# Kernel tuning notes

Hardware: AMD Instinct MI355X
Metric: run time of the kernel (lower is better)

Reference implementation:

```python
import jax, jax.numpy as jnp
import numpy as np
from jax import lax

B, P, ENC = 64, 196, 2048
E, H, A, V = 512, 512, 512, 10000
L = 21  # caption length -> T = 20 decode steps


def setup_inputs() -> dict:
    key = jax.random.key(0)
    ks = jax.random.split(key, 20)
    s = 0.02
    inp = {
        "features": jax.random.normal(ks[0], (B, P, ENC), jnp.float32),
        "captions": jax.random.randint(ks[1], (B, L), 0, V),
        # attention
        "W_enc_att": jax.random.normal(ks[2], (ENC, A), jnp.float32) * s,
        "b_enc_att": jnp.zeros((A,), jnp.float32),
        "W_dec_att": jax.random.normal(ks[3], (H, A), jnp.float32) * s,
        "b_dec_att": jnp.zeros((A,), jnp.float32),
        "W_full": jax.random.normal(ks[4], (A, 1), jnp.float32) * s,
        "b_full": jnp.zeros((1,), jnp.float32),
        # embedding (uniform(-0.1, 0.1) as in init_weights)
        "emb": jax.random.uniform(ks[5], (V, E), jnp.float32, -0.1, 0.1),
        # LSTMCell: input = embed + encoder_dim, gate order i,f,g,o
        "W_ih": jax.random.normal(ks[6], (E + ENC, 4 * H), jnp.float32) * s,
        "W_hh": jax.random.normal(ks[7], (H, 4 * H), jnp.float32) * s,
        "b_ih": jnp.zeros((4 * H,), jnp.float32),
        "b_hh": jnp.zeros((4 * H,), jnp.float32),
        # init state projections
        "W_init_h": jax.random.normal(ks[8], (ENC, H), jnp.float32) * s,
        "b_init_h": jnp.zeros((H,), jnp.float32),
        "W_init_c": jax.random.normal(ks[9], (ENC, H), jnp.float32) * s,
        "b_init_c": jnp.zeros((H,), jnp.float32),
        # gating
        "W_fbeta": jax.random.normal(ks[10], (H, ENC), jnp.float32) * s,
        "b_fbeta": jnp.zeros((ENC,), jnp.float32),
        # output fc (uniform(-0.1,0.1), bias 0)
        "W_fc": jax.random.uniform(ks[11], (H, V), jnp.float32, -0.1, 0.1),
        "b_fc": jnp.zeros((V,), jnp.float32),
    }
    return inp


def reference(features, captions, W_enc_att, b_enc_att, W_dec_att, b_dec_att,
              W_full, b_full, emb, W_ih, W_hh, b_ih, b_hh,
              W_init_h, b_init_h, W_init_c, b_init_c,
              W_fbeta, b_fbeta, W_fc, b_fc):
    # init hidden state from mean-pooled encoder features
    mean_enc = features.mean(axis=1)                       # [B, ENC]
    h0 = mean_enc @ W_init_h + b_init_h                    # [B, H]
    c0 = mean_enc @ W_init_c + b_init_c

    # encoder-side attention projection is time-invariant: precompute
    att1 = features @ W_enc_att + b_enc_att                # [B, P, A]

    T = captions.shape[1] - 1                              # decode_lengths = L-1 (equal lengths)
    embs = emb[captions[:, :T]]                            # [B, T, E]
    embs_t = jnp.swapaxes(embs, 0, 1)                      # [T, B, E]

    def step(carry, e_t):
        h, c = carry
        att2 = h @ W_dec_att + b_dec_att                   # [B, A]
        scores = (jax.nn.relu(att1 + att2[:, None, :]) @ W_full)[..., 0] + b_full  # [B, P]
        alpha = jax.nn.softmax(scores, axis=1)
        awe = jnp.einsum('bp,bpe->be', alpha, features)    # [B, ENC]
        gate = jax.nn.sigmoid(h @ W_fbeta + b_fbeta)
        awe = gate * awe
        x = jnp.concatenate([e_t, awe], axis=1)            # [B, E+ENC]
        gates = x @ W_ih + h @ W_hh + b_ih + b_hh          # [B, 4H]
        i, f, g, o = jnp.split(gates, 4, axis=1)
        c_new = jax.nn.sigmoid(f) * c + jax.nn.sigmoid(i) * jnp.tanh(g)
        h_new = jax.nn.sigmoid(o) * jnp.tanh(c_new)
        preds = h_new @ W_fc + b_fc                        # dropout in eval mode = identity
        return (h_new, c_new), preds

    _, preds = lax.scan(step, (h0, c0), embs_t)            # [T, B, V]
    return jnp.swapaxes(preds, 0, 1)                       # [B, T, V]
```

## Files before the change

### kernel.cpp

```cpp
#include <hip/hip_runtime.h>
#include <hip/hip_bf16.h>


#define TB 256

typedef __bf16 bf16x8 __attribute__((ext_vector_type(8)));
typedef float f32x4 __attribute__((ext_vector_type(4)));
typedef unsigned short u16x8 __attribute__((ext_vector_type(8)));
typedef unsigned short u16x4 __attribute__((ext_vector_type(4)));
typedef unsigned short ushort_t;

__device__ __forceinline__ ushort_t f2bf(float x) {
    unsigned u = __builtin_bit_cast(unsigned, x);
    u += 0x7fffu + ((u >> 16) & 1u);
    return (ushort_t)(u >> 16);
}
__device__ __forceinline__ float bf2f(ushort_t b) {
    return __builtin_bit_cast(float, (unsigned)b << 16);
}
__device__ __forceinline__ void store_pack(
    ushort_t* __restrict__ Ph, ushort_t* __restrict__ Pl,
    int KC, int m, int k, float v)
{
    const size_t flat = ((((size_t)(m >> 4) * KC + (k >> 5)) * 64)
                         + ((k & 31) >> 3) * 16 + (m & 15)) * 8 + (k & 7);
    const ushort_t h = f2bf(v);
    Ph[flat] = h;
    Pl[flat] = f2bf(v - bf2f(h));
}

struct PackJobs {
    const float* W[7];
    ushort_t* Bh[7];
    ushort_t* Bl[7];
    int Nsrc[7], ntCount[7], KC[7], ntBase[7];
    int cum[8];
};

__global__ __launch_bounds__(TB) void pack_all(PackJobs J)
{
    const int blk = blockIdx.x;
    int j = 0;
    #pragma unroll
    for (int i = 1; i < 7; ++i) if (blk >= J.cum[i]) j = i;
    const int g = (blk - J.cum[j]) * TB + threadIdx.x;
    const int KC = J.KC[j];
    const int lane = g & 63;
    const int kc = (g >> 6) % KC;
    const int nt = g / (64 * KC);
    if (nt >= J.ntCount[j]) return;
    const int Nsrc = J.Nsrc[j];
    const float* W = J.W[j];
    const int n = nt * 16 + (lane & 15);
    const int kb = kc * 32 + (lane >> 4) * 8;
    u16x8 hv, lv;
    #pragma unroll
    for (int e = 0; e < 8; ++e) {
        const float x = (n < Nsrc) ? W[(size_t)(kb + e) * Nsrc + n] : 0.f;
        const ushort_t h = f2bf(x);
        hv[e] = h;
        lv[e] = f2bf(x - bf2f(h));
    }
    const size_t flat = (((size_t)(J.ntBase[j] + nt) * KC + kc) * 64 + lane) * 8;
    *(u16x8*)&J.Bh[j][flat] = hv;
    *(u16x8*)&J.Bl[j][flat] = lv;
}

__global__ __launch_bounds__(TB) void feat2bf(
    const float* __restrict__ f, ushort_t* __restrict__ fbf)
{
    const size_t i8 = ((size_t)blockIdx.x * TB + threadIdx.x) * 8;
    const float4 a = *(const float4*)&f[i8];
    const float4 b = *(const float4*)&f[i8 + 4];
    u16x8 v;
    v[0] = f2bf(a.x); v[1] = f2bf(a.y); v[2] = f2bf(a.z); v[3] = f2bf(a.w);
    v[4] = f2bf(b.x); v[5] = f2bf(b.y); v[6] = f2bf(b.z); v[7] = f2bf(b.w);
    *(u16x8*)&fbf[i8] = v;
}

template<int MT, int NT, int WR, int WC>
__device__ __forceinline__ void mfma_tile(
    const ushort_t* lds, int wr, int wc, int lane,
    f32x4 acc[MT / WR][NT / WC])
{
    constexpr int MFR = MT / WR, NFR = NT / WC;
    bf16x8 ah[MFR], al[MFR];
    #pragma unroll
    for (int i = 0; i < MFR; ++i) {
        ah[i] = __builtin_bit_cast(bf16x8, *(const u16x8*)&lds[(wr * MFR + i) * 512 + lane * 8]);
        al[i] = __builtin_bit_cast(bf16x8, *(const u16x8*)&lds[(MT + wr * MFR + i) * 512 + lane * 8]);
    }
    #pragma unroll
    for (int j = 0; j < NFR; ++j) {
        const bf16x8 bh = __builtin_bit_cast(bf16x8, *(const u16x8*)&lds[(2 * MT + wc * NFR + j) * 512 + lane * 8]);
        const bf16x8 bl = __builtin_bit_cast(bf16x8, *(const u16x8*)&lds[(2 * MT + NT + wc * NFR + j) * 512 + lane * 8]);
        #pragma unroll
        for (int i = 0; i < MFR; ++i) {
            acc[i][j] = __builtin_amdgcn_mfma_f32_16x16x32_bf16(ah[i], bh, acc[i][j], 0, 0, 0);
            acc[i][j] = __builtin_amdgcn_mfma_f32_16x16x32_bf16(ah[i], bl, acc[i][j], 0, 0, 0);
            acc[i][j] = __builtin_amdgcn_mfma_f32_16x16x32_bf16(al[i], bh, acc[i][j], 0, 0, 0);
        }
    }
}

template<int MT, int NT, int WR, int WC>
__global__ __launch_bounds__(TB) void gemm_mfma(
    const ushort_t* __restrict__ Ah, const ushort_t* __restrict__ Al,
    const ushort_t* __restrict__ Bh, const ushort_t* __restrict__ Bl,
    int KC, int kcPer,
    const float* __restrict__ bias,
    float* __restrict__ C, int ldc, int Ncols, size_t cPartStride)
{
    constexpr int MFR = MT / WR, NFR = NT / WC, CH = 2 * (MT + NT);
    __shared__ __align__(16) ushort_t lds[CH * 512];
    const int tid = threadIdx.x, wid = tid >> 6, lane = tid & 63;
    const int wr = wid / WC, wc = wid % WC;

    const int tot = gridDim.x * gridDim.y;
    const int lin = blockIdx.x + gridDim.x * blockIdx.y;
    const int q = tot >> 3, r = tot & 7;
    const int xcd = lin & 7, jj = lin >> 3;
    const int base = (xcd < r) ? xcd * (q + 1) : r * (q + 1) + (xcd - r) * q;
    const int lin2 = base + jj;
    const int nb = lin2 / gridDim.y;
    const int mb = lin2 % gridDim.y;

    const int kc0 = blockIdx.z * kcPer;

    f32x4 acc[MFR][NFR];
    #pragma unroll
    for (int i = 0; i < MFR; ++i)
        #pragma unroll
        for (int j = 0; j < NFR; ++j)
            acc[i][j] = f32x4{0.f, 0.f, 0.f, 0.f};

    for (int kc = kc0; kc < kc0 + kcPer; ++kc) {
        __syncthreads();
        #pragma unroll
        for (int cc = 0; cc < CH / 4; ++cc) {
            const int c = cc * 4 + wid;
            const ushort_t* src;
            if (c < MT)                src = Ah + ((size_t)(mb * MT + c) * KC + kc) * 512;
            else if (c < 2 * MT)       src = Al + ((size_t)(mb * MT + c - MT) * KC + kc) * 512;
            else if (c < 2 * MT + NT)  src = Bh + ((size_t)(nb * NT + c - 2 * MT) * KC + kc) * 512;
            else                       src = Bl + ((size_t)(nb * NT + c - 2 * MT - NT) * KC + kc) * 512;
            *(u16x8*)&lds[c * 512 + lane * 8] = *(const u16x8*)(src + lane * 8);
        }
        __syncthreads();
        mfma_tile<MT, NT, WR, WC>(lds, wr, wc, lane, acc);
    }

    C += (size_t)blockIdx.z * cPartStride;
    #pragma unroll
    for (int i = 0; i < MFR; ++i)
        #pragma unroll
        for (int j = 0; j < NFR; ++j) {
            const int col = nb * NT * 16 + (wc * NFR + j) * 16 + (lane & 15);
            if (col < Ncols) {
                const float bv = bias ? bias[col] : 0.f;
                const int rbase = mb * MT * 16 + (wr * MFR + i) * 16 + ((lane >> 4) << 2);
                #pragma unroll
                for (int r2 = 0; r2 < 4; ++r2)
                    C[(size_t)(rbase + r2) * ldc + col] = acc[i][j][r2] + bv;
            }
        }
}

__global__ __launch_bounds__(TB) void gemm_att1(
    const ushort_t* __restrict__ fbf,
    const ushort_t* __restrict__ Bh, const ushort_t* __restrict__ Bl,
    const float* __restrict__ bias, ushort_t* __restrict__ att1bf)
{
    __shared__ __align__(16) ushort_t lds[20 * 512];
    const int tid = threadIdx.x, wid = tid >> 6, lane = tid & 63;
    const int wr = wid >> 1, wc = wid & 1;

    const int lin = blockIdx.x + (blockIdx.y << 2);
    const int lin2 = (lin & 7) * 98 + (lin >> 3);
    const int nb = lin2 & 3, mb = lin2 >> 2;

    f32x4 acc[2][4];
    #pragma unroll
    for (int i = 0; i < 2; ++i)
        #pragma unroll
        for (int j = 0; j < 4; ++j)
            acc[i][j] = f32x4{0.f, 0.f, 0.f, 0.f};

    const int arow = tid >> 2, akg = tid & 3;
    const size_t abase = (size_t)(mb * 64 + arow) * 2048 + akg * 8;
    const int aldst = (arow >> 4) * 512 + (akg * 16 + (arow & 15)) * 8;

    for (int kc = 0; kc < 64; ++kc) {
        __syncthreads();
        #pragma unroll
        for (int cc = 0; cc < 4; ++cc) {
            const int c = cc * 4 + wid;
            const ushort_t* src = (c < 8)
                ? Bh + ((size_t)(nb * 8 + c) * 64 + kc) * 512
                : Bl + ((size_t)(nb * 8 + c - 8) * 64 + kc) * 512;
            *(u16x8*)&lds[(4 + c) * 512 + lane * 8] = *(const u16x8*)(src + lane * 8);
        }
        *(u16x8*)&lds[aldst] = *(const u16x8*)&fbf[abase + (size_t)kc * 32];
        __syncthreads();

        bf16x8 ah[2];
        #pragma unroll
        for (int i = 0; i < 2; ++i)
            ah[i] = __builtin_bit_cast(bf16x8, *(const u16x8*)&lds[(wr * 2 + i) * 512 + lane * 8]);
        #pragma unroll
        for (int j = 0; j < 4; ++j) {
            const bf16x8 bh = __builtin_bit_cast(bf16x8, *(const u16x8*)&lds[(4 + wc * 4 + j) * 512 + lane * 8]);
            const bf16x8 bl = __builtin_bit_cast(bf16x8, *(const u16x8*)&lds[(12 + wc * 4 + j) * 512 + lane * 8]);
            #pragma unroll
            for (int i = 0; i < 2; ++i) {
                acc[i][j] = __builtin_amdgcn_mfma_f32_16x16x32_bf16(ah[i], bh, acc[i][j], 0, 0, 0);
                acc[i][j] = __builtin_amdgcn_mfma_f32_16x16x32_bf16(ah[i], bl, acc[i][j], 0, 0, 0);
            }
        }
    }

    #pragma unroll
    for (int i = 0; i < 2; ++i)
        #pragma unroll
        for (int j = 0; j < 4; ++j) {
            const int col = nb * 128 + (wc * 4 + j) * 16 + (lane & 15);
            const float bv = bias[col];
            const int rbase = mb * 64 + (wr * 2 + i) * 16 + ((lane >> 4) << 2);
            #pragma unroll
            for (int r = 0; r < 4; ++r)
                att1bf[(size_t)(rbase + r) * 512 + col] = f2bf(acc[i][j][r] + bv);
        }
}

__device__ __forceinline__ void gemm_body(
    float (*As)[68], float (*Ws)[68],
    const float* __restrict__ A, int lda,
    const float* __restrict__ W, int ldw,
    float* __restrict__ C, int ldc,
    int nTile, int N, int K)
{
    const int tid = threadIdx.x;
    const int tn = tid & 15;
    const int tm = tid >> 4;
    const int n0 = nTile * 64;

    float acc[4][4] = {{0.f}};

    for (int k0 = 0; k0 < K; k0 += 32) {
        {
            int r  = tid >> 3;
            int cc = (tid & 7) * 4;
            #pragma unroll
            for (int rr = 0; rr < 64; rr += 32) {
                const float4 a = *(const float4*)&A[(size_t)(rr + r) * lda + (k0 + cc)];
                As[cc + 0][rr + r] = a.x;
                As[cc + 1][rr + r] = a.y;
                As[cc + 2][rr + r] = a.z;
                As[cc + 3][rr + r] = a.w;
            }
        }
        {
            int r  = tid >> 4;
            int cc = (tid & 15) * 4;
            #pragma unroll
            for (int rr = 0; rr < 32; rr += 16) {
                const float4 w = *(const float4*)&W[(size_t)(k0 + rr + r) * ldw + (n0 + cc)];
                *(float4*)&Ws[rr + r][cc] = w;
            }
        }
        __syncthreads();
        #pragma unroll
        for (int kk = 0; kk < 32; ++kk) {
            const float4 a = *(const float4*)&As[kk][tm * 4];
            const float4 w = *(const float4*)&Ws[kk][tn * 4];
            const float av[4] = {a.x, a.y, a.z, a.w};
            const float wv[4] = {w.x, w.y, w.z, w.w};
            #pragma unroll
            for (int i = 0; i < 4; ++i)
                #pragma unroll
                for (int j = 0; j < 4; ++j)
                    acc[i][j] = fmaf(av[i], wv[j], acc[i][j]);
        }
        __syncthreads();
    }

    #pragma unroll
    for (int i = 0; i < 4; ++i) {
        const int m = tm * 4 + i;
        #pragma unroll
        for (int j = 0; j < 4; ++j)
            C[(size_t)m * ldc + (n0 + tn * 4 + j)] = acc[i][j];
    }
}

__global__ __launch_bounds__(TB) void gemm_hc(
    const float* __restrict__ mean,
    const float* __restrict__ Wh0, const float* __restrict__ Wc0,
    float* __restrict__ h0p, float* __restrict__ c0p)
{
    __shared__ float As[32][68];
    __shared__ float Ws[32][68];
    const int ks = blockIdx.y & 7;
    const int which = blockIdx.y >> 3;
    const float* W = which ? Wc0 : Wh0;
    float* Cp = which ? c0p : h0p;
    gemm_body(As, Ws,
              mean + (size_t)ks * 256, 2048,
              W + (size_t)ks * 256 * 512, 512,
              Cp + (size_t)ks * 64 * 512, 512,
              blockIdx.x, 512, 256);
}

__global__ __launch_bounds__(TB) void scores_k(
    const ushort_t* __restrict__ att1bf,
    const float* __restrict__ hga_part,
    const float* __restrict__ bd,
    const float* __restrict__ Wfull,
    float* __restrict__ scores)
{
    const int b = blockIdx.x;
    const int tid = threadIdx.x;
    const int wave = tid >> 6;
    const int lane = tid & 63;

    __shared__ float a2[512];
    __shared__ float wf[512];

    for (int i = tid; i < 512; i += TB) {
        float v = bd[i];
        #pragma unroll
        for (int s = 0; s < 4; ++s)
            v += hga_part[(size_t)s * 64 * 4608 + (size_t)b * 4608 + i];
        a2[i] = v;
        wf[i] = Wfull[i];
    }
    __syncthreads();

    const int k0 = lane * 8;
    float a2r[8], wfr[8];
    #pragma unroll
    for (int e = 0; e < 8; ++e) { a2r[e] = a2[k0 + e]; wfr[e] = wf[k0 + e]; }

    const int p0 = blockIdx.y * 28 + wave * 7;
    #pragma unroll
    for (int pp = 0; pp < 7; ++pp) {
        const int p = p0 + pp;
        const u16x8 v = *(const u16x8*)&att1bf[((size_t)b * 196 + p) * 512 + k0];
        float s = 0.f;
        #pragma unroll
        for (int e = 0; e < 8; ++e)
            s = fmaf(fmaxf(bf2f(v[e]) + a2r[e], 0.f), wfr[e], s);
        #pragma unroll
        for (int o = 32; o; o >>= 1) s += __shfl_xor(s, o);
        if (lane == 0) scores[b * 196 + p] = s;
    }
}

__global__ __launch_bounds__(512) void awe_gate(
    const float* __restrict__ scores,
    const ushort_t* __restrict__ fbf,
    const float* __restrict__ hga_part,
    const float* __restrict__ bf,
    ushort_t* __restrict__ gPh, ushort_t* __restrict__ gPl)
{
    const int b = blockIdx.y, chunk = blockIdx.x;
    const int tid = threadIdx.x;
    const int q = tid >> 6, lane = tid & 63;

    __shared__ float al[196];
    __shared__ float redm[8], reds[8];
    __shared__ float smq[8][512];

    const float sv = (tid < 196) ? scores[b * 196 + tid] : -1e30f;
    float m = sv;
    #pragma unroll
    for (int o = 32; o; o >>= 1) m = fmaxf(m, __shfl_xor(m, o));
    if (lane == 0) redm[q] = m;
    __syncthreads();
    m = redm[0];
    #pragma unroll
    for (int i = 1; i < 8; ++i) m = fmaxf(m, redm[i]);

    const float e = (tid < 196) ? expf(sv - m) : 0.f;
    float s = e;
    #pragma unroll
    for (int o = 32; o; o >>= 1) s += __shfl_xor(s, o);
    if (lane == 0) reds[q] = s;
    __syncthreads();
    s = reds[0];
    #pragma unroll
    for (int i = 1; i < 8; ++i) s += reds[i];

    if (tid < 196) al[tid] = e / s;
    __syncthreads();

    const int col0 = chunk * 512 + lane * 8;
    const ushort_t* f = fbf + (size_t)b * 196 * 2048 + col0;
    float acc[8] = {0.f, 0.f, 0.f, 0.f, 0.f, 0.f, 0.f, 0.f};
    const int p0 = q * 25;
    const int pn = (q == 7) ? 21 : 25;
    for (int pp = 0; pp < pn; ++pp) {
        const float w = al[p0 + pp];
        const u16x8 v = *(const u16x8*)&f[(size_t)(p0 + pp) * 2048];
        #pragma unroll
        for (int ee = 0; ee < 8; ++ee)
            acc[ee] = fmaf(w, bf2f(v[ee]), acc[ee]);
    }
    *(f32x4*)&smq[q][lane * 8]     = f32x4{acc[0], acc[1], acc[2], acc[3]};
    *(f32x4*)&smq[q][lane * 8 + 4] = f32x4{acc[4], acc[5], acc[6], acc[7]};
    __syncthreads();

    const int eg = chunk * 512 + tid;
    float a = smq[0][tid];
    #pragma unroll
    for (int i = 1; i < 8; ++i) a += smq[i][tid];
    float gp = bf[eg];
    #pragma unroll
    for (int ss = 0; ss < 4; ++ss)
        gp += hga_part[(size_t)ss * 64 * 4608 + (size_t)b * 4608 + 512 + eg];
    const float gate = 1.f / (1.f + expf(-gp));
    store_pack(gPh, gPl, 64, b, eg, gate * a);
}

__global__ __launch_bounds__(TB) void lstm_pw(
    const float* __restrict__ gates_part,
    const float* __restrict__ hga_part,
    const float* __restrict__ eW,
    const float* __restrict__ b_hh,
    int t,
    float* __restrict__ c,
    ushort_t* __restrict__ hPh, ushort_t* __restrict__ hPl,
    ushort_t* __restrict__ sPh, ushort_t* __restrict__ sPl)
{
    const int idx = blockIdx.x * TB + threadIdx.x;
    const int b = idx >> 9;
    const int j = idx & 511;

    float g[4];
    #pragma unroll
    for (int comp = 0; comp < 4; ++comp) {
        const int col = comp * 512 + j;
        float v = b_hh[col] + eW[((size_t)b * 20 + t) * 2048 + col];
        #pragma unroll
        for (int s = 0; s < 8; ++s)
            v += gates_part[(size_t)s * 64 * 2048 + (size_t)b * 2048 + col];
        #pragma unroll
        for (int s = 0; s < 4; ++s)
            v += hga_part[(size_t)s * 64 * 4608 + (size_t)b * 4608 + 2560 + col];
        g[comp] = v;
    }
    const float si = 1.f / (1.f + expf(-g[0]));
    const float sf = 1.f / (1.f + expf(-g[1]));
    const float gg = tanhf(g[2]);
    const float so = 1.f / (1.f + expf(-g[3]));
    const float cn = sf * c[idx] + si * gg;
    c[idx] = cn;
    const float hn = so * tanhf(cn);
    store_pack(hPh, hPl, 16, b, j, hn);
    store_pack(sPh, sPl, 16, b * 20 + t, j, hn);
}

__global__ __launch_bounds__(TB) void mean_feat(
    const float* __restrict__ features, float* __restrict__ mean_enc)
{
    const int b = blockIdx.y;
    const int e = blockIdx.x * TB + threadIdx.x;
    const float* f = features + (size_t)b * 196 * 2048 + e;
    float s = 0.f;
    #pragma unroll 4
    for (int p = 0; p < 196; ++p) s += f[(size_t)p * 2048];
    mean_enc[b * 2048 + e] = s * (1.f / 196.f);
}

__global__ __launch_bounds__(TB) void gather_emb_pack(
    const int* __restrict__ captions,
    const float* __restrict__ emb,
    ushort_t* __restrict__ Ph, ushort_t* __restrict__ Pl)
{
    const int bt = blockIdx.x;
    const int b = bt / 20;
    const int t = bt % 20;
    const int tok = captions[b * 21 + t];
    for (int e = threadIdx.x; e < 512; e += TB)
        store_pack(Ph, Pl, 16, bt, e, emb[(size_t)tok * 512 + e]);
}

__global__ __launch_bounds__(TB) void reduce_hc(
    const float* __restrict__ h0p, const float* __restrict__ c0p,
    const float* __restrict__ bh0, const float* __restrict__ bc0,
    ushort_t* __restrict__ hPh, ushort_t* __restrict__ hPl,
    float* __restrict__ c)
{
    const int idx = blockIdx.x * TB + threadIdx.x;
    const int half = idx >> 15;
    const int i = idx & 32767;
    const int j = i & 511;
    const float* P = half ? c0p : h0p;
    float v = half ? bc0[j] : bh0[j];
    #pragma unroll
    for (int s = 0; s < 8; ++s) v += P[(size_t)s * 64 * 512 + i];
    if (half) c[i] = v;
    else      store_pack(hPh, hPl, 16, i >> 9, j, v);
}

extern "C" void kernel_launch(void* const* d_in, const int* in_sizes, int n_in,
                              void* d_out, int out_size, void* d_ws, size_t ws_size,
                              hipStream_t stream)
{
    const float* features  = (const float*)d_in[0];
    const int*   captions  = (const int*)  d_in[1];
    const float* W_enc_att = (const float*)d_in[2];
    const float* b_enc_att = (const float*)d_in[3];
    const float* W_dec_att = (const float*)d_in[4];
    const float* b_dec_att = (const float*)d_in[5];
    const float* W_full    = (const float*)d_in[6];
    const float* emb       = (const float*)d_in[8];
    const float* W_ih      = (const float*)d_in[9];
    const float* W_hh      = (const float*)d_in[10];
    const float* b_ih      = (const float*)d_in[11];
    const float* b_hh      = (const float*)d_in[12];
    const float* W_init_h  = (const float*)d_in[13];
    const float* b_init_h  = (const float*)d_in[14];
    const float* W_init_c  = (const float*)d_in[15];
    const float* b_init_c  = (const float*)d_in[16];
    const float* W_fbeta   = (const float*)d_in[17];
    const float* b_fbeta   = (const float*)d_in[18];
    const float* W_fc      = (const float*)d_in[19];
    const float* b_fc      = (const float*)d_in[20];
    float* out = (float*)d_out;
    (void)ws_size;

    float* ws = (float*)d_ws;
    size_t off = 0;
    auto alloc  = [&](size_t n) { float* p = ws + off; off += n; return p; };
    auto ualloc = [&](size_t n) { ushort_t* p = (ushort_t*)(ws + off); off += (n + 1) / 2; return p; };

    float* eW     = alloc((size_t)64 * 20 * 2048);
    float* mean   = alloc(64 * 2048);
    float* hga    = alloc((size_t)4 * 64 * 4608);
    float* gatesp = alloc((size_t)8 * 64 * 2048);
    float* c      = alloc(64 * 512);
    float* scores = alloc(64 * 196);

    ushort_t* fbf    = ualloc((size_t)12544 * 2048);
    ushort_t* att1bf = ualloc((size_t)12544 * 512);
    ushort_t* WencH = ualloc((size_t)32 * 64 * 512);
    ushort_t* WencL = ualloc((size_t)32 * 64 * 512);
    ushort_t* WtopH = ualloc((size_t)128 * 16 * 512);
    ushort_t* WtopL = ualloc((size_t)128 * 16 * 512);
    ushort_t* Wih2H = ualloc((size_t)128 * 64 * 512);
    ushort_t* Wih2L = ualloc((size_t)128 * 64 * 512);
    ushort_t* WdfhH = ualloc((size_t)288 * 16 * 512);
    ushort_t* WdfhL = ualloc((size_t)288 * 16 * 512);
    ushort_t* WfcH  = ualloc((size_t)632 * 16 * 512);
    ushort_t* WfcL  = ualloc((size_t)632 * 16 * 512);
    ushort_t* embsH = ualloc((size_t)80 * 16 * 512);
    ushort_t* embsL = ualloc((size_t)80 * 16 * 512);
    ushort_t* hPh   = ualloc((size_t)4 * 16 * 512);
    ushort_t* hPl   = ualloc((size_t)4 * 16 * 512);
    ushort_t* gPh   = ualloc((size_t)4 * 64 * 512);
    ushort_t* gPl   = ualloc((size_t)4 * 64 * 512);
    ushort_t* sPh   = ualloc((size_t)80 * 16 * 512);
    ushort_t* sPl   = ualloc((size_t)80 * 16 * 512);

    float* h0p = hga;
    float* c0p = gatesp;

    PackJobs J;
    J.W[0]=W_enc_att;               J.Bh[0]=WencH; J.Bl[0]=WencL; J.Nsrc[0]=512;   J.ntCount[0]=32;  J.KC[0]=64; J.ntBase[0]=0;
    J.W[1]=W_ih;                    J.Bh[1]=WtopH; J.Bl[1]=WtopL; J.Nsrc[1]=2048;  J.ntCount[1]=128; J.KC[1]=16; J.ntBase[1]=0;
    J.W[2]=W_ih + (size_t)512*2048; J.Bh[2]=Wih2H; J.Bl[2]=Wih2L; J.Nsrc[2]=2048;  J.ntCount[2]=128; J.KC[2]=64; J.ntBase[2]=0;
    J.W[3]=W_dec_att;               J.Bh[3]=WdfhH; J.Bl[3]=WdfhL; J.Nsrc[3]=512;   J.ntCount[3]=32;  J.KC[3]=16; J.ntBase[3]=0;
    J.W[4]=W_fbeta;                 J.Bh[4]=WdfhH; J.Bl[4]=WdfhL; J.Nsrc[4]=2048;  J.ntCount[4]=128; J.KC[4]=16; J.ntBase[4]=32;
    J.W[5]=W_hh;                    J.Bh[5]=WdfhH; J.Bl[5]=WdfhL; J.Nsrc[5]=2048;  J.ntCount[5]=128; J.KC[5]=16; J.ntBase[5]=160;
    J.W[6]=W_fc;                    J.Bh[6]=WfcH;  J.Bl[6]=WfcL;  J.Nsrc[6]=10000; J.ntCount[6]=632; J.KC[6]=16; J.ntBase[6]=0;
    {
        int cum = 0;
        const int blks[7] = {512, 512, 2048, 128, 512, 512, 2528};
        for (int i = 0; i < 7; ++i) { J.cum[i] = cum; cum += blks[i]; }
        J.cum[7] = cum;
        pack_all<<<cum, TB, 0, stream>>>(J);
    }

    feat2bf<<<12544, TB, 0, stream>>>(features, fbf);
    gather_emb_pack<<<1280, TB, 0, stream>>>(captions, emb, embsH, embsL);
    mean_feat<<<dim3(8, 64), TB, 0, stream>>>(features, mean);
    gemm_hc<<<dim3(8, 16), TB, 0, stream>>>(mean, W_init_h, W_init_c, h0p, c0p);
    reduce_hc<<<256, TB, 0, stream>>>(h0p, c0p, b_init_h, b_init_c, hPh, hPl, c);
    gemm_att1<<<dim3(4, 196), TB, 0, stream>>>(fbf, WencH, WencL, b_enc_att, att1bf);
    gemm_mfma<8, 8, 2, 2><<<dim3(16, 10, 1), TB, 0, stream>>>(
        embsH, embsL, WtopH, WtopL, 16, 16, b_ih, eW, 2048, 2048, 0);

    for (int t = 0; t < 20; ++t) {
        gemm_mfma<4, 8, 2, 2><<<dim3(36, 1, 4), TB, 0, stream>>>(
            hPh, hPl, WdfhH, WdfhL, 16, 4, nullptr, hga, 4608, 4608, (size_t)64 * 4608);
        scores_k<<<dim3(64, 7), TB, 0, stream>>>(att1bf, hga, b_dec_att, W_full, scores);
        awe_gate<<<dim3(4, 64), 512, 0, stream>>>(scores, fbf, hga, b_fbeta, gPh, gPl);
        gemm_mfma<4, 8, 2, 2><<<dim3(16, 1, 8), TB, 0, stream>>>(
            gPh, gPl, Wih2H, Wih2L, 64, 8, nullptr, gatesp, 2048, 2048, (size_t)64 * 2048);
        lstm_pw<<<128, TB, 0, stream>>>(gatesp, hga, eW, b_hh, t, c, hPh, hPl, sPh, sPl);
    }

    gemm_mfma<8, 8, 2, 2><<<dim3(79, 10, 1), TB, 0, stream>>>(
        sPh, sPl, WfcH, WfcL, 16, 16, b_fc, out, 10000, 10000, 0);
}
```

Baseline: 1.056 ms.

## Double-buffer att1 GEMM, fuse scores into attention kernel, widen split-K

The att1 GEMM now uses 128-row tiles with register-staged double-buffered LDS loads, so the next K chunk is fetched while the current one runs on MFMA. The scores and awe_gate kernels are merged into one attention kernel. Each of the 4 column-chunk blocks recomputes the full score vector redundantly, which saves a launch and the scores round trip at the cost of four times the score work. The Wih2 split-K goes from 8 to 16 partial sums, which adds parallelism but makes the LSTM reduction larger. The mean is now computed from the bf16 features, which reads less memory but loses some precision.

```diff
diff --git a/kernel.cpp b/kernel.cpp
--- a/kernel.cpp
+++ b/kernel.cpp
@@ -171,61 +171,90 @@
     const ushort_t* __restrict__ Bh, const ushort_t* __restrict__ Bl,
     const float* __restrict__ bias, ushort_t* __restrict__ att1bf)
 {
-    __shared__ __align__(16) ushort_t lds[20 * 512];
+    __shared__ __align__(16) ushort_t lds[2 * 24 * 512];
     const int tid = threadIdx.x, wid = tid >> 6, lane = tid & 63;
     const int wr = wid >> 1, wc = wid & 1;
 
     const int lin = blockIdx.x + (blockIdx.y << 2);
-    const int lin2 = (lin & 7) * 98 + (lin >> 3);
+    const int lin2 = (lin & 7) * 49 + (lin >> 3);
     const int nb = lin2 & 3, mb = lin2 >> 2;
 
-    f32x4 acc[2][4];
-    #pragma unroll
-    for (int i = 0; i < 2; ++i)
+    f32x4 acc[4][4];
+    #pragma unroll
+    for (int i = 0; i < 4; ++i)
         #pragma unroll
         for (int j = 0; j < 4; ++j)
             acc[i][j] = f32x4{0.f, 0.f, 0.f, 0.f};
 
-    const int arow = tid >> 2, akg = tid & 3;
-    const size_t abase = (size_t)(mb * 64 + arow) * 2048 + akg * 8;
-    const int aldst = (arow >> 4) * 512 + (akg * 16 + (arow & 15)) * 8;
-
-    for (int kc = 0; kc < 64; ++kc) {
-        __syncthreads();
+    u16x8 regs[6];
+
+    auto issue = [&](int kc) {
         #pragma unroll
         for (int cc = 0; cc < 4; ++cc) {
             const int c = cc * 4 + wid;
             const ushort_t* src = (c < 8)
                 ? Bh + ((size_t)(nb * 8 + c) * 64 + kc) * 512
-                : Bl + ((size_t)(nb * 8 + c - 8) * 64 + kc) * 512;
-            *(u16x8*)&lds[(4 + c) * 512 + lane * 8] = *(const u16x8*)(src + lane * 8);
-        }
-        *(u16x8*)&lds[aldst] = *(const u16x8*)&fbf[abase + (size_t)kc * 32];
-        __syncthreads();
-
-        bf16x8 ah[2];
-        #pragma unroll
-        for (int i = 0; i < 2; ++i)
-            ah[i] = __builtin_bit_cast(bf16x8, *(const u16x8*)&lds[(wr * 2 + i) * 512 + lane * 8]);
+                : Bl + ((size_t)(nb * 8 + (c - 8)) * 64 + kc) * 512;
+            regs[cc] = *(const u16x8*)(src + lane * 8);
+        }
+        #pragma unroll
+        for (int p = 0; p < 2; ++p) {
+            const int id = p * 256 + tid;
+            const int row = id >> 2, kg = id & 3;
+            regs[4 + p] = *(const u16x8*)&fbf[(size_t)(mb * 128 + row) * 2048 + (size_t)kc * 32 + kg * 8];
+        }
+    };
+    auto commit = [&](ushort_t* buf) {
+        #pragma unroll
+        for (int cc = 0; cc < 4; ++cc) {
+            const int c = cc * 4 + wid;
+            *(u16x8*)&buf[(8 + c) * 512 + lane * 8] = regs[cc];
+        }
+        #pragma unroll
+        for (int p = 0; p < 2; ++p) {
+            const int id = p * 256 + tid;
+            const int row = id >> 2, kg = id & 3;
+            *(u16x8*)&buf[(row >> 4) * 512 + (kg * 16 + (row & 15)) * 8] = regs[4 + p];
+        }
+    };
+
+    issue(0);
+    commit(lds);
+    __syncthreads();
+
+    int cur = 0;
+    for (int kc = 0; kc < 64; ++kc) {
+        const bool more = (kc + 1 < 64);
+        if (more) issue(kc + 1);
+
+        const ushort_t* buf = lds + cur * 24 * 512;
+        bf16x8 ah[4];
+        #pragma unroll
+        for (int i = 0; i < 4; ++i)
+            ah[i] = __builtin_bit_cast(bf16x8, *(const u16x8*)&buf[(wr * 4 + i) * 512 + lane * 8]);
         #pragma unroll
         for (int j = 0; j < 4; ++j) {
-            const bf16x8 bh = __builtin_bit_cast(bf16x8, *(const u16x8*)&lds[(4 + wc * 4 + j) * 512 + lane * 8]);
-            const bf16x8 bl = __builtin_bit_cast(bf16x8, *(const u16x8*)&lds[(12 + wc * 4 + j) * 512 + lane * 8]);
+            const bf16x8 bh = __builtin_bit_cast(bf16x8, *(const u16x8*)&buf[(8 + wc * 4 + j) * 512 + lane * 8]);
+            const bf16x8 bl = __builtin_bit_cast(bf16x8, *(const u16x8*)&buf[(16 + wc * 4 + j) * 512 + lane * 8]);
             #pragma unroll
-            for (int i = 0; i < 2; ++i) {
+            for (int i = 0; i < 4; ++i) {
                 acc[i][j] = __builtin_amdgcn_mfma_f32_16x16x32_bf16(ah[i], bh, acc[i][j], 0, 0, 0);
                 acc[i][j] = __builtin_amdgcn_mfma_f32_16x16x32_bf16(ah[i], bl, acc[i][j], 0, 0, 0);
             }
         }
-    }
-
-    #pragma unroll
-    for (int i = 0; i < 2; ++i)
+
+        if (more) commit(lds + (cur ^ 1) * 24 * 512);
+        __syncthreads();
+        cur ^= 1;
+    }
+
+    #pragma unroll
+    for (int i = 0; i < 4; ++i)
         #pragma unroll
         for (int j = 0; j < 4; ++j) {
             const int col = nb * 128 + (wc * 4 + j) * 16 + (lane & 15);
             const float bv = bias[col];
-            const int rbase = mb * 64 + (wr * 2 + i) * 16 + ((lane >> 4) << 2);
+            const int rbase = mb * 128 + (wr * 4 + i) * 16 + ((lane >> 4) << 2);
             #pragma unroll
             for (int r = 0; r < 4; ++r)
                 att1bf[(size_t)(rbase + r) * 512 + col] = f2bf(acc[i][j][r] + bv);
@@ -311,39 +340,41 @@
               blockIdx.x, 512, 256);
 }
 
-__global__ __launch_bounds__(TB) void scores_k(
+__global__ __launch_bounds__(512) void attn_fused(
     const ushort_t* __restrict__ att1bf,
-    const float* __restrict__ hga_part,
+    const float* __restrict__ hga,
     const float* __restrict__ bd,
     const float* __restrict__ Wfull,
-    float* __restrict__ scores)
-{
-    const int b = blockIdx.x;
-    const int tid = threadIdx.x;
-    const int wave = tid >> 6;
-    const int lane = tid & 63;
-
-    __shared__ float a2[512];
+    const ushort_t* __restrict__ fbf,
+    const float* __restrict__ bfb,
+    ushort_t* __restrict__ gPh, ushort_t* __restrict__ gPl)
+{
+    const int b = blockIdx.y, chunk = blockIdx.x;
+    const int tid = threadIdx.x, w = tid >> 6, lane = tid & 63;
+
+    __shared__ float att2[512];
     __shared__ float wf[512];
-
-    for (int i = tid; i < 512; i += TB) {
-        float v = bd[i];
+    __shared__ float sc[200];
+    __shared__ float redm[8], reds[8];
+    __shared__ float smq[8][512];
+
+    {
+        float v = bd[tid];
         #pragma unroll
         for (int s = 0; s < 4; ++s)
-            v += hga_part[(size_t)s * 64 * 4608 + (size_t)b * 4608 + i];
-        a2[i] = v;
-        wf[i] = Wfull[i];
+            v += hga[(size_t)s * 64 * 4608 + (size_t)b * 4608 + tid];
+        att2[tid] = v;
+        wf[tid] = Wfull[tid];
     }
     __syncthreads();
 
+    const int p0 = (w < 4) ? w * 25 : 100 + (w - 4) * 24;
+    const int pn = (w < 4) ? 25 : 24;
     const int k0 = lane * 8;
     float a2r[8], wfr[8];
     #pragma unroll
-    for (int e = 0; e < 8; ++e) { a2r[e] = a2[k0 + e]; wfr[e] = wf[k0 + e]; }
-
-    const int p0 = blockIdx.y * 28 + wave * 7;
-    #pragma unroll
-    for (int pp = 0; pp < 7; ++pp) {
+    for (int e = 0; e < 8; ++e) { a2r[e] = att2[k0 + e]; wfr[e] = wf[k0 + e]; }
+    for (int pp = 0; pp < pn; ++pp) {
         const int p = p0 + pp;
         const u16x8 v = *(const u16x8*)&att1bf[((size_t)b * 196 + p) * 512 + k0];
         float s = 0.f;
@@ -352,74 +383,55 @@
             s = fmaf(fmaxf(bf2f(v[e]) + a2r[e], 0.f), wfr[e], s);
         #pragma unroll
         for (int o = 32; o; o >>= 1) s += __shfl_xor(s, o);
-        if (lane == 0) scores[b * 196 + p] = s;
-    }
-}
-
-__global__ __launch_bounds__(512) void awe_gate(
-    const float* __restrict__ scores,
-    const ushort_t* __restrict__ fbf,
-    const float* __restrict__ hga_part,
-    const float* __restrict__ bf,
-    ushort_t* __restrict__ gPh, ushort_t* __restrict__ gPl)
-{
-    const int b = blockIdx.y, chunk = blockIdx.x;
-    const int tid = threadIdx.x;
-    const int q = tid >> 6, lane = tid & 63;
-
-    __shared__ float al[196];
-    __shared__ float redm[8], reds[8];
-    __shared__ float smq[8][512];
-
-    const float sv = (tid < 196) ? scores[b * 196 + tid] : -1e30f;
+        if (lane == 0) sc[p] = s;
+    }
+    __syncthreads();
+
+    const float sv = (tid < 196) ? sc[tid] : -1e30f;
     float m = sv;
     #pragma unroll
     for (int o = 32; o; o >>= 1) m = fmaxf(m, __shfl_xor(m, o));
-    if (lane == 0) redm[q] = m;
+    if (lane == 0) redm[w] = m;
     __syncthreads();
     m = redm[0];
     #pragma unroll
     for (int i = 1; i < 8; ++i) m = fmaxf(m, redm[i]);
-
     const float e = (tid < 196) ? expf(sv - m) : 0.f;
     float s = e;
     #pragma unroll
     for (int o = 32; o; o >>= 1) s += __shfl_xor(s, o);
-    if (lane == 0) reds[q] = s;
+    if (lane == 0) reds[w] = s;
     __syncthreads();
     s = reds[0];
     #pragma unroll
     for (int i = 1; i < 8; ++i) s += reds[i];
-
-    if (tid < 196) al[tid] = e / s;
+    if (tid < 196) sc[tid] = e / s;
     __syncthreads();
 
     const int col0 = chunk * 512 + lane * 8;
     const ushort_t* f = fbf + (size_t)b * 196 * 2048 + col0;
     float acc[8] = {0.f, 0.f, 0.f, 0.f, 0.f, 0.f, 0.f, 0.f};
-    const int p0 = q * 25;
-    const int pn = (q == 7) ? 21 : 25;
     for (int pp = 0; pp < pn; ++pp) {
-        const float w = al[p0 + pp];
+        const float wgt = sc[p0 + pp];
         const u16x8 v = *(const u16x8*)&f[(size_t)(p0 + pp) * 2048];
         #pragma unroll
         for (int ee = 0; ee < 8; ++ee)
-            acc[ee] = fmaf(w, bf2f(v[ee]), acc[ee]);
-    }
-    *(f32x4*)&smq[q][lane * 8]     = f32x4{acc[0], acc[1], acc[2], acc[3]};
-    *(f32x4*)&smq[q][lane * 8 + 4] = f32x4{acc[4], acc[5], acc[6], acc[7]};
+            acc[ee] = fmaf(wgt, bf2f(v[ee]), acc[ee]);
+    }
+    *(f32x4*)&smq[w][lane * 8]     = f32x4{acc[0], acc[1], acc[2], acc[3]};
+    *(f32x4*)&smq[w][lane * 8 + 4] = f32x4{acc[4], acc[5], acc[6], acc[7]};
     __syncthreads();
 
-    const int eg = chunk * 512 + tid;
+    const int cg = chunk * 512 + tid;
     float a = smq[0][tid];
     #pragma unroll
     for (int i = 1; i < 8; ++i) a += smq[i][tid];
-    float gp = bf[eg];
+    float gp = bfb[cg];
     #pragma unroll
     for (int ss = 0; ss < 4; ++ss)
-        gp += hga_part[(size_t)ss * 64 * 4608 + (size_t)b * 4608 + 512 + eg];
+        gp += hga[(size_t)ss * 64 * 4608 + (size_t)b * 4608 + 512 + cg];
     const float gate = 1.f / (1.f + expf(-gp));
-    store_pack(gPh, gPl, 64, b, eg, gate * a);
+    store_pack(gPh, gPl, 64, b, cg, gate * a);
 }
 
 __global__ __launch_bounds__(TB) void lstm_pw(
@@ -442,7 +454,7 @@
         const int col = comp * 512 + j;
         float v = b_hh[col] + eW[((size_t)b * 20 + t) * 2048 + col];
         #pragma unroll
-        for (int s = 0; s < 8; ++s)
+        for (int s = 0; s < 16; ++s)
             v += gates_part[(size_t)s * 64 * 2048 + (size_t)b * 2048 + col];
         #pragma unroll
         for (int s = 0; s < 4; ++s)
@@ -460,15 +472,15 @@
     store_pack(sPh, sPl, 16, b * 20 + t, j, hn);
 }
 
-__global__ __launch_bounds__(TB) void mean_feat(
-    const float* __restrict__ features, float* __restrict__ mean_enc)
+__global__ __launch_bounds__(TB) void mean_feat_bf(
+    const ushort_t* __restrict__ fbf, float* __restrict__ mean_enc)
 {
     const int b = blockIdx.y;
     const int e = blockIdx.x * TB + threadIdx.x;
-    const float* f = features + (size_t)b * 196 * 2048 + e;
+    const ushort_t* f = fbf + (size_t)b * 196 * 2048 + e;
     float s = 0.f;
     #pragma unroll 4
-    for (int p = 0; p < 196; ++p) s += f[(size_t)p * 2048];
+    for (int p = 0; p < 196; ++p) s += bf2f(f[(size_t)p * 2048]);
     mean_enc[b * 2048 + e] = s * (1.f / 196.f);
 }
 
@@ -538,9 +550,8 @@
     float* eW     = alloc((size_t)64 * 20 * 2048);
     float* mean   = alloc(64 * 2048);
     float* hga    = alloc((size_t)4 * 64 * 4608);
-    float* gatesp = alloc((size_t)8 * 64 * 2048);
+    float* gatesp = alloc((size_t)16 * 64 * 2048);
     float* c      = alloc(64 * 512);
-    float* scores = alloc(64 * 196);
 
     ushort_t* fbf    = ualloc((size_t)12544 * 2048);
     ushort_t* att1bf = ualloc((size_t)12544 * 512);
@@ -584,20 +595,20 @@
 
     feat2bf<<<12544, TB, 0, stream>>>(features, fbf);
     gather_emb_pack<<<1280, TB, 0, stream>>>(captions, emb, embsH, embsL);
-    mean_feat<<<dim3(8, 64), TB, 0, stream>>>(features, mean);
+    mean_feat_bf<<<dim3(8, 64), TB, 0, stream>>>(fbf, mean);
     gemm_hc<<<dim3(8, 16), TB, 0, stream>>>(mean, W_init_h, W_init_c, h0p, c0p);
     reduce_hc<<<256, TB, 0, stream>>>(h0p, c0p, b_init_h, b_init_c, hPh, hPl, c);
-    gemm_att1<<<dim3(4, 196), TB, 0, stream>>>(fbf, WencH, WencL, b_enc_att, att1bf);
+    gemm_att1<<<dim3(4, 98), TB, 0, stream>>>(fbf, WencH, WencL, b_enc_att, att1bf);
     gemm_mfma<8, 8, 2, 2><<<dim3(16, 10, 1), TB, 0, stream>>>(
         embsH, embsL, WtopH, WtopL, 16, 16, b_ih, eW, 2048, 2048, 0);
 
     for (int t = 0; t < 20; ++t) {
         gemm_mfma<4, 8, 2, 2><<<dim3(36, 1, 4), TB, 0, stream>>>(
             hPh, hPl, WdfhH, WdfhL, 16, 4, nullptr, hga, 4608, 4608, (size_t)64 * 4608);
-        scores_k<<<dim3(64, 7), TB, 0, stream>>>(att1bf, hga, b_dec_att, W_full, scores);
-        awe_gate<<<dim3(4, 64), 512, 0, stream>>>(scores, fbf, hga, b_fbeta, gPh, gPl);
-        gemm_mfma<4, 8, 2, 2><<<dim3(16, 1, 8), TB, 0, stream>>>(
-            gPh, gPl, Wih2H, Wih2L, 64, 8, nullptr, gatesp, 2048, 2048, (size_t)64 * 2048);
+        attn_fused<<<dim3(4, 64), 512, 0, stream>>>(
+            att1bf, hga, b_dec_att, W_full, fbf, b_fbeta, gPh, gPl);
+        gemm_mfma<4, 8, 2, 2><<<dim3(16, 1, 16), TB, 0, stream>>>(
+            gPh, gPl, Wih2H, Wih2L, 64, 4, nullptr, gatesp, 2048, 2048, (size_t)64 * 2048);
         lstm_pw<<<128, TB, 0, stream>>>(gatesp, hga, eW, b_hh, t, c, hPh, hPl, sPh, sPl);
     }
 
```

Measured after the change: 1.170 ms. 10.8% more time.
